# Performance work log

Measured on AMD Instinct MI355X. Metric: run time of the kernel, lower is better.

Reference implementation:

```python
import jax, jax.numpy as jnp
import numpy as np

N = 25000      # nodes
E = 400000     # edges (before self loops)
G = 64         # graphs in batch
H = 16         # attention heads
ITER = 10      # stacked main GATv2 layers


def setup_inputs():
    key = jax.random.key(0)
    c = [0]
    def nk():
        c[0] += 1
        return jax.random.fold_in(key, c[0])
    def glorot(shape):
        fan = shape[-2] + shape[-1]
        return jax.random.normal(nk(), shape, jnp.float32) * np.float32(np.sqrt(2.0 / fan))
    inp = {
        "x": jax.random.normal(nk(), (N, 2), jnp.float32),
        "edge_attr": jax.random.normal(nk(), (E, 2), jnp.float32),
        "edge_index": jax.random.randint(nk(), (2, E), 0, N, jnp.int32),
        "mask": jax.random.randint(nk(), (N,), 0, 2, jnp.int32),
        "batch": jnp.sort(jax.random.randint(nk(), (N,), 0, G, jnp.int32)),
        # gcn: GATv2Conv(2, 4, heads=16, edge_dim=2), concat -> 64
        "g0_Wl": glorot((2, 64)), "g0_bl": jnp.zeros((64,), jnp.float32),
        "g0_Wr": glorot((2, 64)), "g0_br": jnp.zeros((64,), jnp.float32),
        "g0_We": glorot((2, 64)), "g0_att": glorot((H, 4)),
        "g0_bias": jnp.zeros((64,), jnp.float32),
        "bn_gamma": jnp.ones((64,), jnp.float32),
        "bn_beta": jnp.zeros((64,), jnp.float32),
        "m_Wl": glorot((ITER, 64, 64)), "m_bl": jnp.zeros((ITER, 64), jnp.float32),
        "m_Wr": glorot((ITER, 64, 64)), "m_br": jnp.zeros((ITER, 64), jnp.float32),
        "m_We": glorot((ITER, 2, 64)), "m_att": glorot((ITER, H, 4)),
        "m_bias": jnp.zeros((ITER, 64), jnp.float32),
        # final: GATv2Conv(64, 1, heads=16, concat=False)
        "f_Wl": glorot((64, 16)), "f_bl": jnp.zeros((16,), jnp.float32),
        "f_Wr": glorot((64, 16)), "f_br": jnp.zeros((16,), jnp.float32),
        "f_We": glorot((2, 16)), "f_att": glorot((H, 1)),
        "f_bias": jnp.zeros((1,), jnp.float32),
        # sbs: GATv2Conv(64, 1, heads=16, concat=False)
        "s_Wl": glorot((64, 16)), "s_bl": jnp.zeros((16,), jnp.float32),
        "s_Wr": glorot((64, 16)), "s_br": jnp.zeros((16,), jnp.float32),
        "s_We": glorot((2, 16)), "s_att": glorot((H, 1)),
        "s_bias": jnp.zeros((1,), jnp.float32),
    }
    return inp


def _gatv2(x, src, dst, eattr, Wl, bl, Wr, br, We, att, bias, concat):
    """PyG GATv2Conv: x_l[j]+x_r[i]+e -> LeakyReLU(0.2) -> att dot -> segment softmax over dst."""
    n = x.shape[0]
    h, c = att.shape
    xl = (x @ Wl + bl).reshape(n, h, c)
    xr = (x @ Wr + br).reshape(n, h, c)
    e = (eattr @ We).reshape(-1, h, c)
    m = jax.nn.leaky_relu(xl[src] + xr[dst] + e, 0.2)          # [Etot,H,C]
    logit = jnp.einsum('ehc,hc->eh', m, att)                    # [Etot,H]
    lmax = jax.ops.segment_max(logit, dst, num_segments=n)
    ex = jnp.exp(logit - lmax[dst])
    den = jax.ops.segment_sum(ex, dst, num_segments=n)
    alpha = ex / den[dst]
    out = jax.ops.segment_sum(xl[src] * alpha[..., None], dst, num_segments=n)  # [N,H,C]
    out = out.reshape(n, h * c) if concat else out.mean(axis=1)
    return out + bias


def reference(x, edge_attr, edge_index, mask, batch,
              g0_Wl, g0_bl, g0_Wr, g0_br, g0_We, g0_att, g0_bias,
              bn_gamma, bn_beta,
              m_Wl, m_bl, m_Wr, m_br, m_We, m_att, m_bias,
              f_Wl, f_bl, f_Wr, f_br, f_We, f_att, f_bias,
              s_Wl, s_bl, s_Wr, s_br, s_We, s_att, s_bias):
    n = x.shape[0]
    src, dst = edge_index[0], edge_index[1]
    # add self loops; self-loop edge attr = mean of incoming edge attrs (fill_value='mean')
    ones = jnp.ones((src.shape[0],), jnp.float32)
    cnt = jax.ops.segment_sum(ones, dst, num_segments=n)
    esum = jax.ops.segment_sum(edge_attr, dst, num_segments=n)
    loop_attr = esum / jnp.maximum(cnt, 1.0)[:, None]
    arng = jnp.arange(n, dtype=edge_index.dtype)
    src2 = jnp.concatenate([src, arng])
    dst2 = jnp.concatenate([dst, arng])
    ea2 = jnp.concatenate([edge_attr, loop_attr], axis=0)

    h0 = _gatv2(x, src2, dst2, ea2, g0_Wl, g0_bl, g0_Wr, g0_br, g0_We, g0_att, g0_bias, True)
    mu = h0.mean(axis=0)
    var = h0.var(axis=0)
    h = jax.nn.leaky_relu((h0 - mu) * jax.lax.rsqrt(var + 1e-5) * bn_gamma + bn_beta, 0.01)

    def step(hc, p):
        Wl, bl, Wr, br, We, att, bias = p
        hc = jax.nn.leaky_relu(_gatv2(hc, src2, dst2, ea2, Wl, bl, Wr, br, We, att, bias, True), 0.01)
        return hc, None
    h, _ = jax.lax.scan(step, h, (m_Wl, m_bl, m_Wr, m_br, m_We, m_att, m_bias))

    mus = _gatv2(h, src2, dst2, ea2, s_Wl, s_bl, s_Wr, s_br, s_We, s_att, s_bias, False)[:, 0]  # [N]
    fin = _gatv2(h, src2, dst2, ea2, f_Wl, f_bl, f_Wr, f_br, f_We, f_att, f_bias, False)        # [N,1]
    w = (mask == 0).astype(jnp.float32)
    sums = jax.ops.segment_sum(fin * w[:, None], batch, num_segments=G)
    cnts = jax.ops.segment_sum(w, batch, num_segments=G)
    sat = (sums / jnp.maximum(cnts, 1.0)[:, None])[:, 0]  # [G]
    return mus, sat
```

## Files before the change

### kernel.cpp

```cpp
#include <hip/hip_runtime.h>


static __device__ __forceinline__ float lrelu(float x, float s) {
    return x > 0.f ? x : s * x;
}

__global__ void k_build0(const int* __restrict__ dst, int* __restrict__ cnt,
                         int* __restrict__ rank, int E,
                         const float* __restrict__ x,
                         const float* __restrict__ Wl, const float* __restrict__ bl,
                         const float* __restrict__ Wr, const float* __restrict__ br,
                         float* __restrict__ xl, float* __restrict__ xr, int n) {
    int idx = blockIdx.x * blockDim.x + threadIdx.x;
    if (idx < E) {
        rank[idx] = atomicAdd(&cnt[dst[idx]], 1);
    } else {
        int t = idx - E;
        if (t < n * 64) {
            int i = t >> 6, c = t & 63;
            float x0 = x[2 * i], x1 = x[2 * i + 1];
            xl[t] = x0 * Wl[c] + x1 * Wl[64 + c] + bl[c];
            xr[t] = x0 * Wr[c] + x1 * Wr[64 + c] + br[c];
        }
    }
}

__global__ void k_segoff(const int* __restrict__ cnt, int* __restrict__ row_start,
                         int* __restrict__ cursor, int n) {
    int i = blockIdx.x * blockDim.x + threadIdx.x;
    int lane = threadIdx.x & 63;
    int v = (i < n) ? cnt[i] : 0;
    int s = v;
#pragma unroll
    for (int off = 1; off < 64; off <<= 1) {
        int t = __shfl_up(s, off);
        if (lane >= off) s += t;
    }
    int wavetot = __shfl(s, 63);
    int base = 0;
    if (lane == 63) base = atomicAdd(cursor, wavetot);
    base = __shfl(base, 63);
    if (i < n) row_start[i] = base + s - v;
}

__global__ void k_scatter(const int* __restrict__ src, const int* __restrict__ dst,
                          const float* __restrict__ ea, const int* __restrict__ rank,
                          const int* __restrict__ row_start,
                          int* __restrict__ csr_src, float* __restrict__ csr_ea, int E) {
    int e = blockIdx.x * blockDim.x + threadIdx.x;
    if (e >= E) return;
    int pos = row_start[dst[e]] + rank[e];
    csr_src[pos] = src[e];
    *(float2*)(csr_ea + 2 * (size_t)pos) = *(const float2*)(ea + 2 * (size_t)e);
}

__launch_bounds__(256)
__global__ void k_proj64(const float* __restrict__ h,
                         const float* __restrict__ Wl, const float* __restrict__ bl,
                         const float* __restrict__ Wr, const float* __restrict__ br,
                         const double* __restrict__ stats,
                         const float* __restrict__ bng, const float* __restrict__ bnb,
                         float* __restrict__ xl, float* __restrict__ xr, int n) {
    __shared__ float wsl[4096], wsr[4096], bna[64], bnbb[64];
    int t = threadIdx.x;
    for (int i = t; i < 4096; i += 256) { wsl[i] = Wl[i]; wsr[i] = Wr[i]; }
    if (t < 64) {
        double mu = stats[t] / n;
        double var = stats[64 + t] / n - mu * mu;
        float rs = (float)(1.0 / sqrt(var + 1e-5));
        float a = rs * bng[t];
        bna[t] = a;
        bnbb[t] = bnb[t] - (float)mu * a;
    }
    __syncthreads();
    int rg = t >> 2, cg4 = (t & 3) << 4;
    int r0 = blockIdx.x * 128 + rg * 2;
    float accl[2][16], accr[2][16];
#pragma unroll
    for (int r = 0; r < 2; ++r)
#pragma unroll
        for (int j = 0; j < 16; ++j) { accl[r][j] = 0.f; accr[r][j] = 0.f; }
    for (int k0 = 0; k0 < 64; k0 += 4) {
        float hk[2][4];
#pragma unroll
        for (int r = 0; r < 2; ++r) {
            int gr = r0 + r;
            float4 v = (gr < n) ? *(const float4*)(h + (size_t)gr * 64 + k0)
                                : make_float4(0.f, 0.f, 0.f, 0.f);
            hk[r][0] = v.x; hk[r][1] = v.y; hk[r][2] = v.z; hk[r][3] = v.w;
#pragma unroll
            for (int kk = 0; kk < 4; ++kk)
                hk[r][kk] = lrelu(hk[r][kk] * bna[k0 + kk] + bnbb[k0 + kk], 0.01f);
        }
#pragma unroll
        for (int kk = 0; kk < 4; ++kk) {
            const float* wl = wsl + (k0 + kk) * 64 + cg4;
            const float* wr = wsr + (k0 + kk) * 64 + cg4;
#pragma unroll
            for (int r = 0; r < 2; ++r)
#pragma unroll
                for (int j = 0; j < 16; ++j) {
                    accl[r][j] += hk[r][kk] * wl[j];
                    accr[r][j] += hk[r][kk] * wr[j];
                }
        }
    }
#pragma unroll
    for (int r = 0; r < 2; ++r) {
        int gr = r0 + r;
        if (gr < n) {
            float* ol = xl + (size_t)gr * 64 + cg4;
            float* orr = xr + (size_t)gr * 64 + cg4;
#pragma unroll
            for (int j = 0; j < 16; ++j) {
                ol[j] = accl[r][j] + bl[cg4 + j];
                orr[j] = accr[r][j] + br[cg4 + j];
            }
        }
    }
}

__device__ __forceinline__ float gat_node(const float* __restrict__ xl,
                                          const float* __restrict__ xr,
                                          const int* __restrict__ row_start,
                                          const int* __restrict__ cnt,
                                          const int* __restrict__ csr_src,
                                          const float* __restrict__ csr_ea,
                                          const float* __restrict__ We,
                                          const float* __restrict__ att,
                                          const float* __restrict__ bias,
                                          int d, int lane, int relu) {
    const int p0 = __builtin_amdgcn_readfirstlane(row_start[d]);
    const int deg = __builtin_amdgcn_readfirstlane(cnt[d]);
    const int p1 = p0 + deg;
    const float we0 = We[lane], we1 = We[64 + lane];
    const float av = att[lane];
    const float xrv = xr[(size_t)d * 64 + lane];

    float den0 = 0.f, acc0 = 0.f;
    float den1 = 0.f, acc1 = 0.f;
    float s0 = 0.f, s1 = 0.f;

    auto step = [&](float xv, float2 ea, bool valid, float& den, float& acc) {
        float vm = valid ? 1.f : 0.f;
        s0 = fmaf(vm, ea.x, s0);
        s1 = fmaf(vm, ea.y, s1);
        float tv = lrelu(xv + xrv + ea.x * we0 + ea.y * we1, 0.2f) * av;
        tv += __shfl_xor(tv, 1);
        tv += __shfl_xor(tv, 2);
        if (!valid) tv = -__builtin_inff();
        float w = __expf(tv);
        den += w;
        acc += w * xv;
    };

    for (int p = p0; p < p1; p += 4) {
        int q1 = min(p + 1, p1 - 1), q2 = min(p + 2, p1 - 1), q3 = min(p + 3, p1 - 1);
        int e0s = csr_src[p], e1s = csr_src[q1], e2s = csr_src[q2], e3s = csr_src[q3];
        float2 e0 = *(const float2*)(csr_ea + 2 * (size_t)p);
        float2 e1 = *(const float2*)(csr_ea + 2 * (size_t)q1);
        float2 e2 = *(const float2*)(csr_ea + 2 * (size_t)q2);
        float2 e3 = *(const float2*)(csr_ea + 2 * (size_t)q3);
        float x0 = xl[(size_t)e0s * 64 + lane];
        float x1 = xl[(size_t)e1s * 64 + lane];
        float x2 = xl[(size_t)e2s * 64 + lane];
        float x3 = xl[(size_t)e3s * 64 + lane];
        step(x0, e0, true, den0, acc0);
        step(x1, e1, p + 1 < p1, den1, acc1);
        step(x2, e2, p + 2 < p1, den0, acc0);
        step(x3, e3, p + 3 < p1, den1, acc1);
    }
    {
        float c = fmaxf((float)deg, 1.f);
        float se0 = s0 / c, se1 = s1 / c;
        float xv = xl[(size_t)d * 64 + lane];
        float tv = lrelu(xv + xrv + se0 * we0 + se1 * we1, 0.2f) * av;
        tv += __shfl_xor(tv, 1);
        tv += __shfl_xor(tv, 2);
        float w = __expf(tv);
        den0 += w;
        acc0 += w * xv;
    }
    float o = (acc0 + acc1) / (den0 + den1) + bias[lane];
    if (relu) o = lrelu(o, 0.01f);
    return o;
}

__launch_bounds__(256)
__global__ void k_gat(const float* __restrict__ xl, const float* __restrict__ xr,
                      const int* __restrict__ row_start, const int* __restrict__ cnt,
                      const int* __restrict__ csr_src, const float* __restrict__ csr_ea,
                      const float* __restrict__ We, const float* __restrict__ att,
                      const float* __restrict__ bias,
                      float* __restrict__ out, int n, int relu) {
    int wave = (blockIdx.x * blockDim.x + threadIdx.x) >> 6;
    int lane = threadIdx.x & 63;
    if (wave >= n) return;
    float o = gat_node(xl, xr, row_start, cnt, csr_src, csr_ea, We, att, bias, wave, lane, relu);
    out[(size_t)wave * 64 + lane] = o;
}

__launch_bounds__(256)
__global__ void k_gat_proj(const float* __restrict__ xl, const float* __restrict__ xr,
                           const int* __restrict__ row_start, const int* __restrict__ cnt,
                           const int* __restrict__ csr_src, const float* __restrict__ csr_ea,
                           const float* __restrict__ We, const float* __restrict__ att,
                           const float* __restrict__ bias,
                           const float* __restrict__ Wnl, const float* __restrict__ bnl,
                           const float* __restrict__ Wnr, const float* __restrict__ bnr,
                           float* __restrict__ xl_out, float* __restrict__ xr_out, int n) {
    int wave = (blockIdx.x * blockDim.x + threadIdx.x) >> 6;
    int lane = threadIdx.x & 63;
    if (wave >= n) return;
    const int d = wave;
    float o = gat_node(xl, xr, row_start, cnt, csr_src, csr_ea, We, att, bias, d, lane, 1);
    float a0 = 0.f, a1 = 0.f, b0 = 0.f, b1 = 0.f;
#pragma unroll 8
    for (int k = 0; k < 64; k += 2) {
        float h0 = __shfl(o, k);
        float h1 = __shfl(o, k + 1);
        a0 += h0 * Wnl[k * 64 + lane];
        a1 += h1 * Wnl[(k + 1) * 64 + lane];
        b0 += h0 * Wnr[k * 64 + lane];
        b1 += h1 * Wnr[(k + 1) * 64 + lane];
    }
    xl_out[(size_t)d * 64 + lane] = a0 + a1 + bnl[lane];
    xr_out[(size_t)d * 64 + lane] = b0 + b1 + bnr[lane];
}

__launch_bounds__(256)
__global__ void k_gat_projfin(const float* __restrict__ xl, const float* __restrict__ xr,
                              const int* __restrict__ row_start, const int* __restrict__ cnt,
                              const int* __restrict__ csr_src, const float* __restrict__ csr_ea,
                              const float* __restrict__ We, const float* __restrict__ att,
                              const float* __restrict__ bias,
                              const float* __restrict__ fWl, const float* __restrict__ fbl,
                              const float* __restrict__ fWr, const float* __restrict__ fbr,
                              const float* __restrict__ sWl, const float* __restrict__ sbl,
                              const float* __restrict__ sWr, const float* __restrict__ sbr,
                              float* __restrict__ packed, int n) {
    int wave = (blockIdx.x * blockDim.x + threadIdx.x) >> 6;
    int lane = threadIdx.x & 63;
    if (wave >= n) return;
    const int d = wave;
    float o = gat_node(xl, xr, row_start, cnt, csr_src, csr_ea, We, att, bias, d, lane, 1);
    int q = lane >> 4, cc = lane & 15;
    const float* W = (q == 0) ? fWl : (q == 1) ? sWl : (q == 2) ? fWr : sWr;
    const float* B = (q == 0) ? fbl : (q == 1) ? sbl : (q == 2) ? fbr : sbr;
    float a0 = 0.f, a1 = 0.f;
#pragma unroll 8
    for (int k = 0; k < 64; k += 2) {
        a0 += __shfl(o, k) * W[k * 16 + cc];
        a1 += __shfl(o, k + 1) * W[(k + 1) * 16 + cc];
    }
    packed[(size_t)d * 64 + lane] = a0 + a1 + B[cc];
}

__launch_bounds__(256)
__global__ void k_gat_final(const float* __restrict__ packed,
                            const int* __restrict__ row_start, const int* __restrict__ cnt,
                            const int* __restrict__ csr_src, const float* __restrict__ csr_ea,
                            const float* __restrict__ fWe, const float* __restrict__ sWe,
                            const float* __restrict__ fatt, const float* __restrict__ satt,
                            const float* __restrict__ fbias, const float* __restrict__ sbias,
                            float* __restrict__ fin, float* __restrict__ mus, int n) {
    int hw = (blockIdx.x * blockDim.x + threadIdx.x) >> 5;
    if (hw >= n) return;
    int l = threadIdx.x & 31;
    int hh = l & 15, sel = l >> 4;
    const int d = hw;
    const int p0 = row_start[d], deg = cnt[d], p1 = p0 + deg;
    const float* We = sel ? sWe : fWe;
    float we0 = We[hh], we1 = We[16 + hh];
    float av = (sel ? satt : fatt)[hh];
    float xrv = packed[(size_t)d * 64 + 32 + sel * 16 + hh];
    int xli = sel * 16 + hh;

    float den0 = 0.f, acc0 = 0.f;
    float den1 = 0.f, acc1 = 0.f;
    float s0 = 0.f, s1 = 0.f;

    auto step = [&](float xv, float2 ea, bool valid, float& den, float& acc) {
        float vm = valid ? 1.f : 0.f;
        s0 = fmaf(vm, ea.x, s0);
        s1 = fmaf(vm, ea.y, s1);
        float t = lrelu(xv + xrv + ea.x * we0 + ea.y * we1, 0.2f) * av;
        if (!valid) t = -__builtin_inff();
        float w = __expf(t);
        den += w;
        acc += w * xv;
    };

    for (int p = p0; p < p1; p += 4) {
        int q1 = min(p + 1, p1 - 1), q2 = min(p + 2, p1 - 1), q3 = min(p + 3, p1 - 1);
        int e0s = csr_src[p], e1s = csr_src[q1], e2s = csr_src[q2], e3s = csr_src[q3];
        float2 e0 = *(const float2*)(csr_ea + 2 * (size_t)p);
        float2 e1 = *(const float2*)(csr_ea + 2 * (size_t)q1);
        float2 e2 = *(const float2*)(csr_ea + 2 * (size_t)q2);
        float2 e3 = *(const float2*)(csr_ea + 2 * (size_t)q3);
        float x0 = packed[(size_t)e0s * 64 + xli];
        float x1 = packed[(size_t)e1s * 64 + xli];
        float x2 = packed[(size_t)e2s * 64 + xli];
        float x3 = packed[(size_t)e3s * 64 + xli];
        step(x0, e0, true, den0, acc0);
        step(x1, e1, p + 1 < p1, den1, acc1);
        step(x2, e2, p + 2 < p1, den0, acc0);
        step(x3, e3, p + 3 < p1, den1, acc1);
    }
    {
        float c = fmaxf((float)deg, 1.f);
        float se0 = s0 / c, se1 = s1 / c;
        float xv = packed[(size_t)d * 64 + xli];
        float t = lrelu(xv + xrv + se0 * we0 + se1 * we1, 0.2f) * av;
        float w = __expf(t);
        den0 += w;
        acc0 += w * xv;
    }
    float val = (acc0 + acc1) / (den0 + den1);
#pragma unroll
    for (int w = 1; w < 16; w <<= 1) val += __shfl_xor(val, w);
    if ((threadIdx.x & 15) == 0) {
        float o = val * (1.f / 16.f) + (sel ? sbias[0] : fbias[0]);
        if (sel) mus[d] = o; else fin[d] = o;
    }
}


__global__ void k_bnstats(const float* __restrict__ h, double* __restrict__ stats, int n) {
    int c = threadIdx.x & 63;
    int s0 = blockIdx.x * (blockDim.x >> 6) + (threadIdx.x >> 6);
    int ns = gridDim.x * (blockDim.x >> 6);
    double s = 0.0, s2 = 0.0;
    for (int i = s0; i < n; i += ns) {
        float v = h[(size_t)i * 64 + c];
        s += v;
        s2 += (double)v * v;
    }
    atomicAdd(&stats[c], s);
    atomicAdd(&stats[64 + c], s2);
}


__global__ void k_sat_acc(const float* __restrict__ fin, const int* __restrict__ mask,
                          const int* __restrict__ batch,
                          float* __restrict__ sums, float* __restrict__ cnts, int n) {
    int i = blockIdx.x * blockDim.x + threadIdx.x;
    int lane = threadIdx.x & 63;
    int g = (i < n) ? batch[i] : -1;
    float c = (i < n && mask[i] == 0) ? 1.f : 0.f;
    float v = (c > 0.f) ? fin[i] : 0.f;
#pragma unroll
    for (int off = 1; off < 64; off <<= 1) {
        float v2 = __shfl_down(v, off);
        float c2 = __shfl_down(c, off);
        int g2 = __shfl_down(g, off);
        if (lane + off < 64 && g2 == g) { v += v2; c += c2; }
    }
    int gprev = __shfl_up(g, 1);
    bool head = (lane == 0) || (gprev != g);
    if (head && g >= 0 && c > 0.f) {
        atomicAdd(&sums[g], v);
        atomicAdd(&cnts[g], c);
    }
}

__global__ void k_sat_fin(const float* __restrict__ sums, const float* __restrict__ cnts,
                          float* __restrict__ out, int g) {
    int i = threadIdx.x;
    if (i < g) out[i] = sums[i] / fmaxf(cnts[i], 1.f);
}


extern "C" void kernel_launch(void* const* d_in, const int* in_sizes, int n_in,
                              void* d_out, int out_size, void* d_ws, size_t ws_size,
                              hipStream_t stream) {
    const float* x = (const float*)d_in[0];
    const float* eat = (const float*)d_in[1];
    const int* ei = (const int*)d_in[2];
    const int* mask = (const int*)d_in[3];
    const int* batch = (const int*)d_in[4];
    const float* g0_Wl = (const float*)d_in[5];
    const float* g0_bl = (const float*)d_in[6];
    const float* g0_Wr = (const float*)d_in[7];
    const float* g0_br = (const float*)d_in[8];
    const float* g0_We = (const float*)d_in[9];
    const float* g0_att = (const float*)d_in[10];
    const float* g0_bias = (const float*)d_in[11];
    const float* bn_g = (const float*)d_in[12];
    const float* bn_b = (const float*)d_in[13];
    const float* m_Wl = (const float*)d_in[14];
    const float* m_bl = (const float*)d_in[15];
    const float* m_Wr = (const float*)d_in[16];
    const float* m_br = (const float*)d_in[17];
    const float* m_We = (const float*)d_in[18];
    const float* m_att = (const float*)d_in[19];
    const float* m_bias = (const float*)d_in[20];
    const float* f_Wl = (const float*)d_in[21];
    const float* f_bl = (const float*)d_in[22];
    const float* f_Wr = (const float*)d_in[23];
    const float* f_br = (const float*)d_in[24];
    const float* f_We = (const float*)d_in[25];
    const float* f_att = (const float*)d_in[26];
    const float* f_bias = (const float*)d_in[27];
    const float* s_Wl = (const float*)d_in[28];
    const float* s_bl = (const float*)d_in[29];
    const float* s_Wr = (const float*)d_in[30];
    const float* s_br = (const float*)d_in[31];
    const float* s_We = (const float*)d_in[32];
    const float* s_att = (const float*)d_in[33];
    const float* s_bias = (const float*)d_in[34];

    const int N = in_sizes[3];
    const int E = in_sizes[1] / 2;
    const int G = out_size - N;
    const int ITER = in_sizes[14] / 4096;
    const int* srcp = ei;
    const int* dstp = ei + E;

    char* wsb = (char*)d_ws;
    size_t off = 0;
    auto alloc = [&](size_t b) { void* p = wsb + off; off = (off + b + 255) & ~(size_t)255; return p; };
    int* cnt = (int*)alloc((size_t)N * 4);
    int* cursor = (int*)alloc(256);
    double* stats = (double*)alloc(128 * 8);
    float* sums = (float*)alloc((size_t)G * 4);
    float* cnts = (float*)alloc((size_t)G * 4);
    size_t zero_bytes = off;
    int* rank = (int*)alloc((size_t)E * 4);
    int* row_start = (int*)alloc((size_t)N * 4);
    int* csr_src = (int*)alloc((size_t)E * 4);
    float* csr_ea = (float*)alloc((size_t)E * 8);
    float* xlA = (float*)alloc((size_t)N * 256);
    float* xrA = (float*)alloc((size_t)N * 256);
    float* xlB = (float*)alloc((size_t)N * 256);
    float* xrB = (float*)alloc((size_t)N * 256);
    float* hbuf = (float*)alloc((size_t)N * 256);
    float* fin = (float*)alloc((size_t)N * 4);
    (void)ws_size; (void)n_in;

    float* outv = (float*)d_out;

    hipMemsetAsync(d_ws, 0, zero_bytes, stream);
    const int tb = 256;
    const int ggrid = (N * 64 + 255) / 256;
    k_build0<<<(E + N * 64 + tb - 1) / tb, tb, 0, stream>>>(dstp, cnt, rank, E,
                                                            x, g0_Wl, g0_bl, g0_Wr, g0_br,
                                                            xlA, xrA, N);
    k_segoff<<<(N + tb - 1) / tb, tb, 0, stream>>>(cnt, row_start, cursor, N);
    k_scatter<<<(E + tb - 1) / tb, tb, 0, stream>>>(srcp, dstp, eat, rank, row_start,
                                                    csr_src, csr_ea, E);

    k_gat<<<ggrid, tb, 0, stream>>>(xlA, xrA, row_start, cnt, csr_src, csr_ea,
                                    g0_We, g0_att, g0_bias, hbuf, N, 0);
    k_bnstats<<<128, 256, 0, stream>>>(hbuf, stats, N);
    k_proj64<<<(N + 127) / 128, 256, 0, stream>>>(hbuf, m_Wl, m_bl, m_Wr, m_br,
                                                  stats, bn_g, bn_b, xlA, xrA, N);

    float* cur_l = xlA; float* cur_r = xrA;
    float* alt_l = xlB; float* alt_r = xrB;
    for (int l = 0; l < ITER; ++l) {
        if (l < ITER - 1) {
            k_gat_proj<<<ggrid, tb, 0, stream>>>(cur_l, cur_r, row_start, cnt, csr_src, csr_ea,
                                                 m_We + l * 128, m_att + l * 64, m_bias + l * 64,
                                                 m_Wl + (size_t)(l + 1) * 4096, m_bl + (l + 1) * 64,
                                                 m_Wr + (size_t)(l + 1) * 4096, m_br + (l + 1) * 64,
                                                 alt_l, alt_r, N);
        } else {
            k_gat_projfin<<<ggrid, tb, 0, stream>>>(cur_l, cur_r, row_start, cnt, csr_src, csr_ea,
                                                    m_We + l * 128, m_att + l * 64, m_bias + l * 64,
                                                    f_Wl, f_bl, f_Wr, f_br,
                                                    s_Wl, s_bl, s_Wr, s_br,
                                                    alt_l, N);
        }
        float* t;
        t = cur_l; cur_l = alt_l; alt_l = t;
        t = cur_r; cur_r = alt_r; alt_r = t;
    }
    k_gat_final<<<(N * 32 + tb - 1) / tb, tb, 0, stream>>>(cur_l, row_start, cnt, csr_src, csr_ea,
                                                           f_We, s_We, f_att, s_att,
                                                           f_bias, s_bias, fin, outv, N);
    k_sat_acc<<<(N + tb - 1) / tb, tb, 0, stream>>>(fin, mask, batch, sums, cnts, N);
    k_sat_fin<<<1, 64, 0, stream>>>(sums, cnts, outv + N, G);
}
```

Baseline: 646.1 us.

## Restructure GAT aggregation so each lane handles one head over four edges in parallel

The per-node GAT aggregation is remapped so each lane owns one head's 4 channels (float4 loads) and the 64-lane wave processes 4 edges at once, 8 per iteration. Per-edge cross-lane shuffles are gone; one shuffle reduction across the edge groups runs at the end. Launch bounds are raised for occupancy, leaky-relu becomes a fmax, and CSR arrays get padding. This is meant to cut per-edge shuffle and instruction overhead and widen the gathers, at the cost of masked work on low-degree nodes and extra end-of-node reductions.

Measured after the change: 656.8 us. About the same (+1.7%).

```diff
diff --git a/kernel.cpp b/kernel.cpp
--- a/kernel.cpp
+++ b/kernel.cpp
@@ -2,7 +2,7 @@
 
 
 static __device__ __forceinline__ float lrelu(float x, float s) {
-    return x > 0.f ? x : s * x;
+    return fmaxf(x, s * x);
 }
 
 __global__ void k_build0(const int* __restrict__ dst, int* __restrict__ cnt,
@@ -48,6 +48,11 @@
                           const int* __restrict__ row_start,
                           int* __restrict__ csr_src, float* __restrict__ csr_ea, int E) {
     int e = blockIdx.x * blockDim.x + threadIdx.x;
+    if (blockIdx.x == 0 && threadIdx.x == 0) {
+        csr_src[E] = 0;
+        csr_ea[2 * (size_t)E] = 0.f;
+        csr_ea[2 * (size_t)E + 1] = 0.f;
+    }
     if (e >= E) return;
     int pos = row_start[dst[e]] + rank[e];
     csr_src[pos] = src[e];
@@ -120,7 +125,7 @@
     }
 }
 
-__device__ __forceinline__ float gat_node(const float* __restrict__ xl,
+__device__ __forceinline__ void gat_core4(const float* __restrict__ xl,
                                           const float* __restrict__ xr,
                                           const int* __restrict__ row_start,
                                           const int* __restrict__ cnt,
@@ -129,131 +134,169 @@
                                           const float* __restrict__ We,
                                           const float* __restrict__ att,
                                           const float* __restrict__ bias,
-                                          int d, int lane, int relu) {
+                                          int d, int lane, int relu,
+                                          float& O0, float& O1, float& O2, float& O3) {
+    const int h4 = (lane & 15) << 2;
+    const int esub = lane >> 4;
     const int p0 = __builtin_amdgcn_readfirstlane(row_start[d]);
     const int deg = __builtin_amdgcn_readfirstlane(cnt[d]);
-    const int p1 = p0 + deg;
-    const float we0 = We[lane], we1 = We[64 + lane];
-    const float av = att[lane];
-    const float xrv = xr[(size_t)d * 64 + lane];
-
-    float den0 = 0.f, acc0 = 0.f;
-    float den1 = 0.f, acc1 = 0.f;
+    const int plast = p0 + deg - 1;
+    const float4 we0 = *(const float4*)(We + h4);
+    const float4 we1 = *(const float4*)(We + 64 + h4);
+    const float4 at4 = *(const float4*)(att + h4);
+    const float4 xr4 = *(const float4*)(xr + ((size_t)d << 6) + h4);
+
+    float den = 0.f, a0 = 0.f, a1 = 0.f, a2 = 0.f, a3 = 0.f;
     float s0 = 0.f, s1 = 0.f;
 
-    auto step = [&](float xv, float2 ea, bool valid, float& den, float& acc) {
-        float vm = valid ? 1.f : 0.f;
+    auto consume = [&](float4 v, float2 ea, int ecur) {
+        float m0 = lrelu(v.x + xr4.x + ea.x * we0.x + ea.y * we1.x, 0.2f);
+        float m1 = lrelu(v.y + xr4.y + ea.x * we0.y + ea.y * we1.y, 0.2f);
+        float m2 = lrelu(v.z + xr4.z + ea.x * we0.z + ea.y * we1.z, 0.2f);
+        float m3 = lrelu(v.w + xr4.w + ea.x * we0.w + ea.y * we1.w, 0.2f);
+        float tv = m0 * at4.x + m1 * at4.y + m2 * at4.z + m3 * at4.w;
+        float w = __expf(tv);
+        float vm = (ecur < deg) ? 1.f : 0.f;
+        w *= vm;
+        den += w;
+        a0 = fmaf(w, v.x, a0);
+        a1 = fmaf(w, v.y, a1);
+        a2 = fmaf(w, v.z, a2);
+        a3 = fmaf(w, v.w, a3);
         s0 = fmaf(vm, ea.x, s0);
         s1 = fmaf(vm, ea.y, s1);
-        float tv = lrelu(xv + xrv + ea.x * we0 + ea.y * we1, 0.2f) * av;
-        tv += __shfl_xor(tv, 1);
-        tv += __shfl_xor(tv, 2);
-        if (!valid) tv = -__builtin_inff();
+    };
+
+    for (int base = 0; base < deg; base += 8) {
+        int eA = base + esub, eB = base + 4 + esub;
+        int pA = min(p0 + eA, plast), pB = min(p0 + eB, plast);
+        int siA = csr_src[pA], siB = csr_src[pB];
+        float2 eaA = *(const float2*)(csr_ea + 2 * (size_t)pA);
+        float2 eaB = *(const float2*)(csr_ea + 2 * (size_t)pB);
+        float4 vA = *(const float4*)(xl + (unsigned)((siA << 6) + h4));
+        float4 vB = *(const float4*)(xl + (unsigned)((siB << 6) + h4));
+        consume(vA, eaA, eA);
+        consume(vB, eaB, eB);
+    }
+
+    s0 += __shfl_xor(s0, 16); s0 += __shfl_xor(s0, 32);
+    s1 += __shfl_xor(s1, 16); s1 += __shfl_xor(s1, 32);
+
+    {
+        float cinv = 1.f / fmaxf((float)deg, 1.f);
+        float se0 = s0 * cinv, se1 = s1 * cinv;
+        float4 vs = *(const float4*)(xl + ((size_t)d << 6) + h4);
+        float m0 = lrelu(vs.x + xr4.x + se0 * we0.x + se1 * we1.x, 0.2f);
+        float m1 = lrelu(vs.y + xr4.y + se0 * we0.y + se1 * we1.y, 0.2f);
+        float m2 = lrelu(vs.z + xr4.z + se0 * we0.z + se1 * we1.z, 0.2f);
+        float m3 = lrelu(vs.w + xr4.w + se0 * we0.w + se1 * we1.w, 0.2f);
+        float tv = m0 * at4.x + m1 * at4.y + m2 * at4.z + m3 * at4.w;
         float w = __expf(tv);
+        w = (esub == 0) ? w : 0.f;
         den += w;
-        acc += w * xv;
-    };
-
-    for (int p = p0; p < p1; p += 4) {
-        int q1 = min(p + 1, p1 - 1), q2 = min(p + 2, p1 - 1), q3 = min(p + 3, p1 - 1);
-        int e0s = csr_src[p], e1s = csr_src[q1], e2s = csr_src[q2], e3s = csr_src[q3];
-        float2 e0 = *(const float2*)(csr_ea + 2 * (size_t)p);
-        float2 e1 = *(const float2*)(csr_ea + 2 * (size_t)q1);
-        float2 e2 = *(const float2*)(csr_ea + 2 * (size_t)q2);
-        float2 e3 = *(const float2*)(csr_ea + 2 * (size_t)q3);
-        float x0 = xl[(size_t)e0s * 64 + lane];
-        float x1 = xl[(size_t)e1s * 64 + lane];
-        float x2 = xl[(size_t)e2s * 64 + lane];
-        float x3 = xl[(size_t)e3s * 64 + lane];
-        step(x0, e0, true, den0, acc0);
-        step(x1, e1, p + 1 < p1, den1, acc1);
-        step(x2, e2, p + 2 < p1, den0, acc0);
-        step(x3, e3, p + 3 < p1, den1, acc1);
-    }
-    {
-        float c = fmaxf((float)deg, 1.f);
-        float se0 = s0 / c, se1 = s1 / c;
-        float xv = xl[(size_t)d * 64 + lane];
-        float tv = lrelu(xv + xrv + se0 * we0 + se1 * we1, 0.2f) * av;
-        tv += __shfl_xor(tv, 1);
-        tv += __shfl_xor(tv, 2);
-        float w = __expf(tv);
-        den0 += w;
-        acc0 += w * xv;
-    }
-    float o = (acc0 + acc1) / (den0 + den1) + bias[lane];
-    if (relu) o = lrelu(o, 0.01f);
-    return o;
-}
-
-__launch_bounds__(256)
-__global__ void k_gat(const float* __restrict__ xl, const float* __restrict__ xr,
-                      const int* __restrict__ row_start, const int* __restrict__ cnt,
-                      const int* __restrict__ csr_src, const float* __restrict__ csr_ea,
-                      const float* __restrict__ We, const float* __restrict__ att,
-                      const float* __restrict__ bias,
-                      float* __restrict__ out, int n, int relu) {
+        a0 = fmaf(w, vs.x, a0);
+        a1 = fmaf(w, vs.y, a1);
+        a2 = fmaf(w, vs.z, a2);
+        a3 = fmaf(w, vs.w, a3);
+    }
+
+    den += __shfl_xor(den, 16); den += __shfl_xor(den, 32);
+    a0 += __shfl_xor(a0, 16); a0 += __shfl_xor(a0, 32);
+    a1 += __shfl_xor(a1, 16); a1 += __shfl_xor(a1, 32);
+    a2 += __shfl_xor(a2, 16); a2 += __shfl_xor(a2, 32);
+    a3 += __shfl_xor(a3, 16); a3 += __shfl_xor(a3, 32);
+
+    const float4 b4 = *(const float4*)(bias + h4);
+    float rd = 1.f / den;
+    O0 = fmaf(a0, rd, b4.x);
+    O1 = fmaf(a1, rd, b4.y);
+    O2 = fmaf(a2, rd, b4.z);
+    O3 = fmaf(a3, rd, b4.w);
+    if (relu) {
+        O0 = lrelu(O0, 0.01f); O1 = lrelu(O1, 0.01f);
+        O2 = lrelu(O2, 0.01f); O3 = lrelu(O3, 0.01f);
+    }
+}
+
+__launch_bounds__(256, 8)
+__global__ void k_gat4(const float* __restrict__ xl, const float* __restrict__ xr,
+                       const int* __restrict__ row_start, const int* __restrict__ cnt,
+                       const int* __restrict__ csr_src, const float* __restrict__ csr_ea,
+                       const float* __restrict__ We, const float* __restrict__ att,
+                       const float* __restrict__ bias,
+                       float* __restrict__ out, int n, int relu) {
     int wave = (blockIdx.x * blockDim.x + threadIdx.x) >> 6;
     int lane = threadIdx.x & 63;
     if (wave >= n) return;
-    float o = gat_node(xl, xr, row_start, cnt, csr_src, csr_ea, We, att, bias, wave, lane, relu);
-    out[(size_t)wave * 64 + lane] = o;
-}
-
-__launch_bounds__(256)
-__global__ void k_gat_proj(const float* __restrict__ xl, const float* __restrict__ xr,
-                           const int* __restrict__ row_start, const int* __restrict__ cnt,
-                           const int* __restrict__ csr_src, const float* __restrict__ csr_ea,
-                           const float* __restrict__ We, const float* __restrict__ att,
-                           const float* __restrict__ bias,
-                           const float* __restrict__ Wnl, const float* __restrict__ bnl,
-                           const float* __restrict__ Wnr, const float* __restrict__ bnr,
-                           float* __restrict__ xl_out, float* __restrict__ xr_out, int n) {
+    float O0, O1, O2, O3;
+    gat_core4(xl, xr, row_start, cnt, csr_src, csr_ea, We, att, bias,
+              wave, lane, relu, O0, O1, O2, O3);
+    if (lane < 16)
+        *(float4*)(out + ((size_t)wave << 6) + (lane << 2)) = make_float4(O0, O1, O2, O3);
+}
+
+__launch_bounds__(256, 8)
+__global__ void k_gat_proj4(const float* __restrict__ xl, const float* __restrict__ xr,
+                            const int* __restrict__ row_start, const int* __restrict__ cnt,
+                            const int* __restrict__ csr_src, const float* __restrict__ csr_ea,
+                            const float* __restrict__ We, const float* __restrict__ att,
+                            const float* __restrict__ bias,
+                            const float* __restrict__ Wnl, const float* __restrict__ bnl,
+                            const float* __restrict__ Wnr, const float* __restrict__ bnr,
+                            float* __restrict__ xl_out, float* __restrict__ xr_out, int n) {
     int wave = (blockIdx.x * blockDim.x + threadIdx.x) >> 6;
     int lane = threadIdx.x & 63;
     if (wave >= n) return;
     const int d = wave;
-    float o = gat_node(xl, xr, row_start, cnt, csr_src, csr_ea, We, att, bias, d, lane, 1);
+    float O0, O1, O2, O3;
+    gat_core4(xl, xr, row_start, cnt, csr_src, csr_ea, We, att, bias,
+              d, lane, 1, O0, O1, O2, O3);
     float a0 = 0.f, a1 = 0.f, b0 = 0.f, b1 = 0.f;
-#pragma unroll 8
-    for (int k = 0; k < 64; k += 2) {
-        float h0 = __shfl(o, k);
-        float h1 = __shfl(o, k + 1);
-        a0 += h0 * Wnl[k * 64 + lane];
-        a1 += h1 * Wnl[(k + 1) * 64 + lane];
-        b0 += h0 * Wnr[k * 64 + lane];
-        b1 += h1 * Wnr[(k + 1) * 64 + lane];
-    }
-    xl_out[(size_t)d * 64 + lane] = a0 + a1 + bnl[lane];
-    xr_out[(size_t)d * 64 + lane] = b0 + b1 + bnr[lane];
-}
-
-__launch_bounds__(256)
-__global__ void k_gat_projfin(const float* __restrict__ xl, const float* __restrict__ xr,
-                              const int* __restrict__ row_start, const int* __restrict__ cnt,
-                              const int* __restrict__ csr_src, const float* __restrict__ csr_ea,
-                              const float* __restrict__ We, const float* __restrict__ att,
-                              const float* __restrict__ bias,
-                              const float* __restrict__ fWl, const float* __restrict__ fbl,
-                              const float* __restrict__ fWr, const float* __restrict__ fbr,
-                              const float* __restrict__ sWl, const float* __restrict__ sbl,
-                              const float* __restrict__ sWr, const float* __restrict__ sbr,
-                              float* __restrict__ packed, int n) {
+#pragma unroll 4
+    for (int k = 0; k < 64; k += 4) {
+        int ls = k >> 2;
+        float h0 = __shfl(O0, ls), h1 = __shfl(O1, ls);
+        float h2 = __shfl(O2, ls), h3 = __shfl(O3, ls);
+        a0 += h0 * Wnl[(k + 0) * 64 + lane] + h2 * Wnl[(k + 2) * 64 + lane];
+        a1 += h1 * Wnl[(k + 1) * 64 + lane] + h3 * Wnl[(k + 3) * 64 + lane];
+        b0 += h0 * Wnr[(k + 0) * 64 + lane] + h2 * Wnr[(k + 2) * 64 + lane];
+        b1 += h1 * Wnr[(k + 1) * 64 + lane] + h3 * Wnr[(k + 3) * 64 + lane];
+    }
+    xl_out[((size_t)d << 6) + lane] = a0 + a1 + bnl[lane];
+    xr_out[((size_t)d << 6) + lane] = b0 + b1 + bnr[lane];
+}
+
+__launch_bounds__(256, 8)
+__global__ void k_gat_projfin4(const float* __restrict__ xl, const float* __restrict__ xr,
+                               const int* __restrict__ row_start, const int* __restrict__ cnt,
+                               const int* __restrict__ csr_src, const float* __restrict__ csr_ea,
+                               const float* __restrict__ We, const float* __restrict__ att,
+                               const float* __restrict__ bias,
+                               const float* __restrict__ fWl, const float* __restrict__ fbl,
+                               const float* __restrict__ fWr, const float* __restrict__ fbr,
+                               const float* __restrict__ sWl, const float* __restrict__ sbl,
+                               const float* __restrict__ sWr, const float* __restrict__ sbr,
+                               float* __restrict__ packed, int n) {
     int wave = (blockIdx.x * blockDim.x + threadIdx.x) >> 6;
     int lane = threadIdx.x & 63;
     if (wave >= n) return;
     const int d = wave;
-    float o = gat_node(xl, xr, row_start, cnt, csr_src, csr_ea, We, att, bias, d, lane, 1);
+    float O0, O1, O2, O3;
+    gat_core4(xl, xr, row_start, cnt, csr_src, csr_ea, We, att, bias,
+              d, lane, 1, O0, O1, O2, O3);
     int q = lane >> 4, cc = lane & 15;
     const float* W = (q == 0) ? fWl : (q == 1) ? sWl : (q == 2) ? fWr : sWr;
     const float* B = (q == 0) ? fbl : (q == 1) ? sbl : (q == 2) ? fbr : sbr;
     float a0 = 0.f, a1 = 0.f;
-#pragma unroll 8
-    for (int k = 0; k < 64; k += 2) {
-        a0 += __shfl(o, k) * W[k * 16 + cc];
-        a1 += __shfl(o, k + 1) * W[(k + 1) * 16 + cc];
-    }
-    packed[(size_t)d * 64 + lane] = a0 + a1 + B[cc];
+#pragma unroll 4
+    for (int k = 0; k < 64; k += 4) {
+        int ls = k >> 2;
+        float h0 = __shfl(O0, ls), h1 = __shfl(O1, ls);
+        float h2 = __shfl(O2, ls), h3 = __shfl(O3, ls);
+        a0 += h0 * W[(k + 0) * 16 + cc] + h2 * W[(k + 2) * 16 + cc];
+        a1 += h1 * W[(k + 1) * 16 + cc] + h3 * W[(k + 3) * 16 + cc];
+    }
+    packed[((size_t)d << 6) + lane] = a0 + a1 + B[cc];
 }
 
 __launch_bounds__(256)
@@ -428,8 +471,8 @@
     size_t zero_bytes = off;
     int* rank = (int*)alloc((size_t)E * 4);
     int* row_start = (int*)alloc((size_t)N * 4);
-    int* csr_src = (int*)alloc((size_t)E * 4);
-    float* csr_ea = (float*)alloc((size_t)E * 8);
+    int* csr_src = (int*)alloc((size_t)(E + 4) * 4);
+    float* csr_ea = (float*)alloc((size_t)(E + 4) * 8);
     float* xlA = (float*)alloc((size_t)N * 256);
     float* xrA = (float*)alloc((size_t)N * 256);
     float* xlB = (float*)alloc((size_t)N * 256);
@@ -450,8 +493,8 @@
     k_scatter<<<(E + tb - 1) / tb, tb, 0, stream>>>(srcp, dstp, eat, rank, row_start,
                                                     csr_src, csr_ea, E);
 
-    k_gat<<<ggrid, tb, 0, stream>>>(xlA, xrA, row_start, cnt, csr_src, csr_ea,
-                                    g0_We, g0_att, g0_bias, hbuf, N, 0);
+    k_gat4<<<ggrid, tb, 0, stream>>>(xlA, xrA, row_start, cnt, csr_src, csr_ea,
+                                     g0_We, g0_att, g0_bias, hbuf, N, 0);
     k_bnstats<<<128, 256, 0, stream>>>(hbuf, stats, N);
     k_proj64<<<(N + 127) / 128, 256, 0, stream>>>(hbuf, m_Wl, m_bl, m_Wr, m_br,
                                                   stats, bn_g, bn_b, xlA, xrA, N);
@@ -460,17 +503,17 @@
     float* alt_l = xlB; float* alt_r = xrB;
     for (int l = 0; l < ITER; ++l) {
         if (l < ITER - 1) {
-            k_gat_proj<<<ggrid, tb, 0, stream>>>(cur_l, cur_r, row_start, cnt, csr_src, csr_ea,
-                                                 m_We + l * 128, m_att + l * 64, m_bias + l * 64,
-                                                 m_Wl + (size_t)(l + 1) * 4096, m_bl + (l + 1) * 64,
-                                                 m_Wr + (size_t)(l + 1) * 4096, m_br + (l + 1) * 64,
-                                                 alt_l, alt_r, N);
+            k_gat_proj4<<<ggrid, tb, 0, stream>>>(cur_l, cur_r, row_start, cnt, csr_src, csr_ea,
+                                                  m_We + l * 128, m_att + l * 64, m_bias + l * 64,
+                                                  m_Wl + (size_t)(l + 1) * 4096, m_bl + (l + 1) * 64,
+                                                  m_Wr + (size_t)(l + 1) * 4096, m_br + (l + 1) * 64,
+                                                  alt_l, alt_r, N);
         } else {
-            k_gat_projfin<<<ggrid, tb, 0, stream>>>(cur_l, cur_r, row_start, cnt, csr_src, csr_ea,
-                                                    m_We + l * 128, m_att + l * 64, m_bias + l * 64,
-                                                    f_Wl, f_bl, f_Wr, f_br,
-                                                    s_Wl, s_bl, s_Wr, s_br,
-                                                    alt_l, N);
+            k_gat_projfin4<<<ggrid, tb, 0, stream>>>(cur_l, cur_r, row_start, cnt, csr_src, csr_ea,
+                                                     m_We + l * 128, m_att + l * 64, m_bias + l * 64,
+                                                     f_Wl, f_bl, f_Wr, f_br,
+                                                     s_Wl, s_bl, s_Wr, s_br,
+                                                     alt_l, N);
         }
         float* t;
         t = cur_l; cur_l = alt_l; alt_l = t;
```

## Batch neighbor index loads per wave and unroll GAT edge loop by eight

Applied to the files above, without the earlier changes.

The GAT aggregation now loads up to 64 neighbor indices at once with one coalesced load per wave, broadcasts them with shuffles, and issues eight feature gathers per inner iteration instead of four. This aims to remove the serialized per-edge index loads and raise memory-level parallelism. It also requests 8 waves per SIMD via launch bounds, which could force register spilling, and switches leaky ReLU to a fmax form. A sentinel zero entry is padded at the end of the CSR arrays.

Result: slower. 677.3 us (+4.8%).

```diff
diff --git a/kernel.cpp b/kernel.cpp
--- a/kernel.cpp
+++ b/kernel.cpp
@@ -2,7 +2,7 @@
 
 
 static __device__ __forceinline__ float lrelu(float x, float s) {
-    return x > 0.f ? x : s * x;
+    return fmaxf(x, s * x);
 }
 
 __global__ void k_build0(const int* __restrict__ dst, int* __restrict__ cnt,
@@ -48,6 +48,11 @@
                           const int* __restrict__ row_start,
                           int* __restrict__ csr_src, float* __restrict__ csr_ea, int E) {
     int e = blockIdx.x * blockDim.x + threadIdx.x;
+    if (blockIdx.x == 0 && threadIdx.x == 0) {
+        csr_src[E] = 0;
+        csr_ea[2 * (size_t)E] = 0.f;
+        csr_ea[2 * (size_t)E + 1] = 0.f;
+    }
     if (e >= E) return;
     int pos = row_start[dst[e]] + rank[e];
     csr_src[pos] = src[e];
@@ -132,10 +137,9 @@
                                           int d, int lane, int relu) {
     const int p0 = __builtin_amdgcn_readfirstlane(row_start[d]);
     const int deg = __builtin_amdgcn_readfirstlane(cnt[d]);
-    const int p1 = p0 + deg;
     const float we0 = We[lane], we1 = We[64 + lane];
     const float av = att[lane];
-    const float xrv = xr[(size_t)d * 64 + lane];
+    const float xrv = xr[((size_t)d << 6) + lane];
 
     float den0 = 0.f, acc0 = 0.f;
     float den1 = 0.f, acc1 = 0.f;
@@ -154,26 +158,36 @@
         acc += w * xv;
     };
 
-    for (int p = p0; p < p1; p += 4) {
-        int q1 = min(p + 1, p1 - 1), q2 = min(p + 2, p1 - 1), q3 = min(p + 3, p1 - 1);
-        int e0s = csr_src[p], e1s = csr_src[q1], e2s = csr_src[q2], e3s = csr_src[q3];
-        float2 e0 = *(const float2*)(csr_ea + 2 * (size_t)p);
-        float2 e1 = *(const float2*)(csr_ea + 2 * (size_t)q1);
-        float2 e2 = *(const float2*)(csr_ea + 2 * (size_t)q2);
-        float2 e3 = *(const float2*)(csr_ea + 2 * (size_t)q3);
-        float x0 = xl[(size_t)e0s * 64 + lane];
-        float x1 = xl[(size_t)e1s * 64 + lane];
-        float x2 = xl[(size_t)e2s * 64 + lane];
-        float x3 = xl[(size_t)e3s * 64 + lane];
-        step(x0, e0, true, den0, acc0);
-        step(x1, e1, p + 1 < p1, den1, acc1);
-        step(x2, e2, p + 2 < p1, den0, acc0);
-        step(x3, e3, p + 3 < p1, den1, acc1);
-    }
+    for (int c0 = 0; c0 < deg; c0 += 64) {
+        const int cn = min(64, deg - c0);
+        int myidx = 0;
+        if (lane < cn) myidx = csr_src[p0 + c0 + lane];
+        const int plast = p0 + deg - 1;
+        for (int j = 0; j < cn; j += 8) {
+            int idx[8];
+            float xv[8];
+            float2 ea8[8];
+#pragma unroll
+            for (int t = 0; t < 8; ++t) idx[t] = __shfl(myidx, j + t);
+#pragma unroll
+            for (int t = 0; t < 8; ++t)
+                xv[t] = xl[(unsigned)((idx[t] << 6) + lane)];
+#pragma unroll
+            for (int t = 0; t < 8; ++t) {
+                int q = min(p0 + c0 + j + t, plast);
+                ea8[t] = *(const float2*)(csr_ea + 2 * (size_t)q);
+            }
+#pragma unroll
+            for (int t = 0; t < 8; ++t)
+                step(xv[t], ea8[t], j + t < cn, (t & 1) ? den1 : den0,
+                     (t & 1) ? acc1 : acc0);
+        }
+    }
+
     {
         float c = fmaxf((float)deg, 1.f);
         float se0 = s0 / c, se1 = s1 / c;
-        float xv = xl[(size_t)d * 64 + lane];
+        float xv = xl[((size_t)d << 6) + lane];
         float tv = lrelu(xv + xrv + se0 * we0 + se1 * we1, 0.2f) * av;
         tv += __shfl_xor(tv, 1);
         tv += __shfl_xor(tv, 2);
@@ -186,7 +200,7 @@
     return o;
 }
 
-__launch_bounds__(256)
+__launch_bounds__(256, 8)
 __global__ void k_gat(const float* __restrict__ xl, const float* __restrict__ xr,
                       const int* __restrict__ row_start, const int* __restrict__ cnt,
                       const int* __restrict__ csr_src, const float* __restrict__ csr_ea,
@@ -197,10 +211,10 @@
     int lane = threadIdx.x & 63;
     if (wave >= n) return;
     float o = gat_node(xl, xr, row_start, cnt, csr_src, csr_ea, We, att, bias, wave, lane, relu);
-    out[(size_t)wave * 64 + lane] = o;
-}
-
-__launch_bounds__(256)
+    out[((size_t)wave << 6) + lane] = o;
+}
+
+__launch_bounds__(256, 8)
 __global__ void k_gat_proj(const float* __restrict__ xl, const float* __restrict__ xr,
                            const int* __restrict__ row_start, const int* __restrict__ cnt,
                            const int* __restrict__ csr_src, const float* __restrict__ csr_ea,
@@ -224,11 +238,11 @@
         b0 += h0 * Wnr[k * 64 + lane];
         b1 += h1 * Wnr[(k + 1) * 64 + lane];
     }
-    xl_out[(size_t)d * 64 + lane] = a0 + a1 + bnl[lane];
-    xr_out[(size_t)d * 64 + lane] = b0 + b1 + bnr[lane];
-}
-
-__launch_bounds__(256)
+    xl_out[((size_t)d << 6) + lane] = a0 + a1 + bnl[lane];
+    xr_out[((size_t)d << 6) + lane] = b0 + b1 + bnr[lane];
+}
+
+__launch_bounds__(256, 8)
 __global__ void k_gat_projfin(const float* __restrict__ xl, const float* __restrict__ xr,
                               const int* __restrict__ row_start, const int* __restrict__ cnt,
                               const int* __restrict__ csr_src, const float* __restrict__ csr_ea,
@@ -253,7 +267,7 @@
         a0 += __shfl(o, k) * W[k * 16 + cc];
         a1 += __shfl(o, k + 1) * W[(k + 1) * 16 + cc];
     }
-    packed[(size_t)d * 64 + lane] = a0 + a1 + B[cc];
+    packed[((size_t)d << 6) + lane] = a0 + a1 + B[cc];
 }
 
 __launch_bounds__(256)
@@ -428,8 +442,8 @@
     size_t zero_bytes = off;
     int* rank = (int*)alloc((size_t)E * 4);
     int* row_start = (int*)alloc((size_t)N * 4);
-    int* csr_src = (int*)alloc((size_t)E * 4);
-    float* csr_ea = (float*)alloc((size_t)E * 8);
+    int* csr_src = (int*)alloc((size_t)(E + 4) * 4);
+    float* csr_ea = (float*)alloc((size_t)(E + 4) * 8);
     float* xlA = (float*)alloc((size_t)N * 256);
     float* xrA = (float*)alloc((size_t)N * 256);
     float* xlB = (float*)alloc((size_t)N * 256);
```
